# Optimization experiments

Hardware: AMD Instinct MI355X
Metric: run time of the kernel (lower is better)

The kernel has to match this reference:

```python
import jax, jax.numpy as jnp
import numpy as np

N = 100000
E = 1000000
P = 1000000
HID = 128
ROLE_VOCAB = 8
ROLE_DIM = 16
IDX_VOCAB = 1024
IDX_DIM = 8
FEAT = 14
IN_DIM = FEAT + IDX_DIM + ROLE_DIM  # 38


def setup_inputs() -> dict:
    key = jax.random.key(0)
    ks = jax.random.split(key, 20)
    s = 0.02
    return {
        "block_features": jax.random.normal(ks[0], (N, FEAT), jnp.float32),
        "role_ids": jax.random.randint(ks[1], (N,), 0, ROLE_VOCAB),
        "b2b_src": jax.random.randint(ks[2], (E,), 0, N),
        "b2b_dst": jax.random.randint(ks[3], (E,), 0, N),
        "b2b_w": jax.random.uniform(ks[4], (E,), jnp.float32),
        "p2b_block": jax.random.randint(ks[5], (P,), 0, N),
        "p2b_w": jax.random.uniform(ks[6], (P,), jnp.float32),
        "role_emb": jax.random.normal(ks[7], (ROLE_VOCAB, ROLE_DIM), jnp.float32),
        "idx_emb": jax.random.normal(ks[8], (IDX_VOCAB, IDX_DIM), jnp.float32),
        "W1": jax.random.normal(ks[9], (IN_DIM, HID), jnp.float32) * s,
        "b1": jnp.zeros((HID,), jnp.float32),
        "W2": jax.random.normal(ks[10], (HID, HID), jnp.float32) * s,
        "b2": jnp.zeros((HID,), jnp.float32),
        "M1": jax.random.normal(ks[11], (HID, HID), jnp.float32) * s,
        "mb1": jnp.zeros((HID,), jnp.float32),
        "M2": jax.random.normal(ks[12], (HID, HID), jnp.float32) * s,
        "mb2": jnp.zeros((HID,), jnp.float32),
        "ln_g": jnp.ones((HID,), jnp.float32),
        "ln_b": jnp.zeros((HID,), jnp.float32),
    }


def _layernorm(x, g, b, eps=1e-5):
    mu = jnp.mean(x, axis=-1, keepdims=True)
    var = jnp.mean(jnp.square(x - mu), axis=-1, keepdims=True)
    return (x - mu) * jax.lax.rsqrt(var + eps) * g + b


def reference(block_features, role_ids, b2b_src, b2b_dst, b2b_w, p2b_block, p2b_w,
              role_emb, idx_emb, W1, b1, W2, b2, M1, mb1, M2, mb2, ln_g, ln_b):
    n = block_features.shape[0]
    # embeddings + input MLP
    re = role_emb[role_ids]                                  # [N, 16]
    ie = idx_emb[jnp.arange(n) % IDX_VOCAB]                  # [N, 8]
    x = jnp.concatenate([block_features, re, ie], axis=-1)   # [N, 38]
    h = jax.nn.relu(x @ W1 + b1)
    emb = jax.nn.relu(h @ W2 + b2)                           # [N, HID]
    # b2b: symmetric weighted scatter-add of neighbor embeddings
    agg = jnp.zeros_like(emb)
    agg = agg.at[b2b_src].add(emb[b2b_dst] * b2b_w[:, None])
    agg = agg.at[b2b_dst].add(emb[b2b_src] * b2b_w[:, None])
    # p2b: agg[j] += emb[j] * w  ==  emb * (sum of pin weights per block)
    pw = jnp.zeros((n,), emb.dtype).at[p2b_block].add(p2b_w)
    agg = agg + emb * pw[:, None]
    # message MLP + residual + LayerNorm
    m = jax.nn.relu(agg @ M1 + mb1) @ M2 + mb2
    block_embeddings = _layernorm(emb + m, ln_g, ln_b)
    graph_embedding = jnp.mean(block_embeddings, axis=0)
    return block_embeddings, graph_embedding
```

## Files before the change

kernel.cpp:

```cpp
#include <hip/hip_runtime.h>

#define FEAT 14
#define ROLE_DIM 16
#define IDX_DIM 8
#define IN_DIM 38
#define HID 128
#define IDX_VOCAB 1024
#define BINN 128
#define NBINS_MAX 800
#define NSEG 1024
#define BINP_CAPT 8
#define BINP_SCAP 16
#define SORT_CAP 4096
#define SENT 0xFFFFFFFFu

typedef __attribute__((ext_vector_type(8))) short short8;
typedef __attribute__((ext_vector_type(4))) float f32x4;
typedef __attribute__((ext_vector_type(2))) float f32x2;

__device__ __forceinline__ ushort f2bf(float f) {
    uint u = __float_as_uint(f);
    return (ushort)((u + 0x7FFFu + ((u >> 16) & 1u)) >> 16);
}
__device__ __forceinline__ float bf2f(ushort h) {
    return __uint_as_float((uint)h << 16);
}
__device__ __forceinline__ uchar f2fp8(float f) {
    return (uchar)(__builtin_amdgcn_cvt_pk_fp8_f32(f, f, 0, false) & 0xff);
}

__global__ void k_prep(const float* __restrict__ W1, const float* __restrict__ W2,
                       const float* __restrict__ M1, const float* __restrict__ M2,
                       ushort* __restrict__ W1t, ushort* __restrict__ W2t,
                       ushort* __restrict__ M1t, ushort* __restrict__ M2t)
{
    int t = blockIdx.x * 256 + threadIdx.x;
    if (t < 8192) {
        int c = t >> 6, k = t & 63;
        W1t[t] = (k < IN_DIM) ? f2bf(W1[k * HID + c]) : (ushort)0;
    } else if (t < 24576) {
        int u = t - 8192; int c = u >> 7, k = u & 127;
        W2t[u] = f2bf(W2[k * HID + c]);
    } else if (t < 40960) {
        int u = t - 24576; int c = u >> 7, k = u & 127;
        M1t[u] = f2bf(M1[k * HID + c]);
    } else if (t < 57344) {
        int u = t - 40960; int c = u >> 7, k = u & 127;
        M2t[u] = f2bf(M2[k * HID + c]);
    }
}

#define LDSA 32768

__device__ __forceinline__ void embed_body(
    char* lds, int id,
    const float* __restrict__ feat, const int* __restrict__ role_ids,
    const float* __restrict__ role_emb, const float* __restrict__ idx_emb,
    const ushort* __restrict__ W1t, const float* __restrict__ b1,
    const ushort* __restrict__ W2t, const float* __restrict__ b2,
    ushort* __restrict__ embh, uchar* __restrict__ embf8, int N)
{
    const int tid = threadIdx.x;
    const int w = tid >> 6, l = tid & 63;
    const int li = l & 15, hi = l >> 4;
    const int base = id * 64;

    for (int c = 0; c < 4; ++c) {
        int idx = c * 256 + tid;
        int col = idx >> 3, ch = idx & 7;
        uint4 v = *(const uint4*)(W1t + col * 64 + ch * 8);
        *(uint4*)(lds + col * 256 + ((ch * 16) ^ ((col & 7) << 4))) = v;
    }
    {
        int row = tid >> 2, kq = (tid & 3) * 16;
        int gr = base + row; if (gr >= N) gr = N - 1;
        int rid = role_ids[gr];
        float xv[16];
        #pragma unroll
        for (int j = 0; j < 16; ++j) {
            int k = kq + j;
            float v = 0.0f;
            if (k < FEAT)                 v = feat[gr * FEAT + k];
            else if (k < FEAT + ROLE_DIM) v = role_emb[rid * ROLE_DIM + (k - FEAT)];
            else if (k < IN_DIM)          v = idx_emb[(gr & (IDX_VOCAB - 1)) * IDX_DIM + (k - FEAT - ROLE_DIM)];
            xv[j] = v;
        }
        uint p[8];
        #pragma unroll
        for (int j = 0; j < 8; ++j)
            p[j] = (uint)f2bf(xv[2 * j]) | ((uint)f2bf(xv[2 * j + 1]) << 16);
        char* db = lds + LDSA + row * 256;
        int sw = (row & 7) << 4;
        *(uint4*)(db + ((kq * 2) ^ sw))      = make_uint4(p[0], p[1], p[2], p[3]);
        *(uint4*)(db + ((kq * 2 + 16) ^ sw)) = make_uint4(p[4], p[5], p[6], p[7]);
    }
    __syncthreads();

    f32x4 C[8];
    #pragma unroll
    for (int ct = 0; ct < 8; ++ct) C[ct] = (f32x4){0.f, 0.f, 0.f, 0.f};
    {
        const int arow = w * 16 + li;
        const int asw = (arow & 7) << 4;
        #pragma unroll
        for (int ks = 0; ks < 2; ++ks) {
            short8 a = *(short8*)(lds + LDSA + arow * 256 + ((ks * 64 + hi * 16) ^ asw));
            #pragma unroll
            for (int ct = 0; ct < 8; ++ct) {
                int bcol = ct * 16 + li;
                short8 b = *(short8*)(lds + bcol * 256 + ((ks * 64 + hi * 16) ^ ((bcol & 7) << 4)));
                C[ct] = __builtin_amdgcn_mfma_f32_16x16x32_bf16(a, b, C[ct], 0, 0, 0);
            }
        }
    }
    __syncthreads();

    #pragma unroll
    for (int ct = 0; ct < 8; ++ct) {
        int col = ct * 16 + li;
        float bv = b1[col];
        #pragma unroll
        for (int r = 0; r < 4; ++r) {
            int hrow = w * 16 + hi * 4 + r;
            float h = fmaxf(C[ct][r] + bv, 0.0f);
            *(ushort*)(lds + LDSA + hrow * 256 + ((col * 2) ^ ((hrow & 7) << 4))) = f2bf(h);
        }
    }
    for (int c = 0; c < 8; ++c) {
        int idx = c * 256 + tid;
        int col = idx >> 4, ch = idx & 15;
        uint4 v = *(const uint4*)(W2t + col * 128 + ch * 8);
        *(uint4*)(lds + col * 256 + ((ch * 16) ^ ((col & 7) << 4))) = v;
    }
    __syncthreads();

    f32x4 C2[8];
    #pragma unroll
    for (int ct = 0; ct < 8; ++ct) C2[ct] = (f32x4){0.f, 0.f, 0.f, 0.f};
    {
        const int arow = w * 16 + li;
        const int asw = (arow & 7) << 4;
        #pragma unroll
        for (int ks = 0; ks < 4; ++ks) {
            short8 a = *(short8*)(lds + LDSA + arow * 256 + ((ks * 64 + hi * 16) ^ asw));
            #pragma unroll
            for (int ct = 0; ct < 8; ++ct) {
                int bcol = ct * 16 + li;
                short8 b = *(short8*)(lds + bcol * 256 + ((ks * 64 + hi * 16) ^ ((bcol & 7) << 4)));
                C2[ct] = __builtin_amdgcn_mfma_f32_16x16x32_bf16(a, b, C2[ct], 0, 0, 0);
            }
        }
    }

    #pragma unroll
    for (int ct = 0; ct < 8; ++ct) {
        int col = ct * 16 + li;
        float bv = b2[col];
        #pragma unroll
        for (int r = 0; r < 4; ++r) {
            int gr = base + w * 16 + hi * 4 + r;
            if (gr < N) {
                float o = fmaxf(C2[ct][r] + bv, 0.0f);
                embh[(size_t)gr * 128 + col] = f2bf(o);
                embf8[(size_t)gr * 128 + col] = f2fp8(o);
            }
        }
    }
}

__device__ __forceinline__ void binp_body(
    char* lds, int id,
    const int* __restrict__ src, const int* __restrict__ dst,
    const float* __restrict__ wgt, uint* __restrict__ staged,
    const int* __restrict__ pb, const float* __restrict__ pv,
    float* __restrict__ pw,
    int E, int P, int nbins, int chunkE, int chunkP)
{
    uint* buf   = (uint*)lds;
    int* curT   = (int*)(lds + 25600);
    const int tid = threadIdx.x;
    for (int i = tid; i < nbins; i += 256) curT[i] = 0;
    __syncthreads();

    const int lo = id * chunkE;
    const int hiE = (lo + chunkE) < E ? (lo + chunkE) : E;
    for (int i = lo + tid; i < hiE; i += 256) {
        int s = src[i], d = dst[i];
        uint q = (uint)(wgt[i] * 255.0f + 0.5f);
        int bs = s >> 7;
        uint es = ((uint)(s & 127) << 25) | ((uint)d << 8) | q;
        int ps = atomicAdd(&curT[bs], 1);
        if (ps < BINP_CAPT) buf[bs * BINP_CAPT + ps] = es;
        else if (ps < BINP_SCAP)
            staged[((size_t)bs * NSEG + id) * BINP_SCAP + ps] = es;
        int bd = d >> 7;
        uint ed = ((uint)(d & 127) << 25) | ((uint)s << 8) | q;
        int pd = atomicAdd(&curT[bd], 1);
        if (pd < BINP_CAPT) buf[bd * BINP_CAPT + pd] = ed;
        else if (pd < BINP_SCAP)
            staged[((size_t)bd * NSEG + id) * BINP_SCAP + pd] = ed;
    }
    __syncthreads();
    for (int b = tid; b < nbins; b += 256) {
        int tot = curT[b];
        int k = tot < BINP_CAPT ? tot : BINP_CAPT;
        uint* dp = staged + ((size_t)b * NSEG + id) * BINP_SCAP;
        for (int i = 0; i < k; ++i) dp[i] = buf[b * BINP_CAPT + i];
        if (tot < BINP_SCAP) dp[tot] = SENT;
    }

    int loP = id * chunkP;
    int hiP = loP + chunkP; if (hiP > P) hiP = P;
    for (int i = loP + tid; i < hiP; i += 256)
        atomicAdd(&pw[pb[i]], pv[i]);
}

__global__ __launch_bounds__(256) void k_embed_binp(
    const float* __restrict__ feat, const int* __restrict__ role_ids,
    const float* __restrict__ role_emb, const float* __restrict__ idx_emb,
    const ushort* __restrict__ W1t, const float* __restrict__ b1,
    const ushort* __restrict__ W2t, const float* __restrict__ b2,
    ushort* __restrict__ embh, uchar* __restrict__ embf8,
    const int* __restrict__ src, const int* __restrict__ dst,
    const float* __restrict__ wgt, uint* __restrict__ staged,
    const int* __restrict__ pb, const float* __restrict__ pv,
    float* __restrict__ pw,
    int N, int E, int P, int nbins, int chunkE, int chunkP)
{
    __shared__ char lds[49152];
    const int bid = blockIdx.x;
    int role, id;
    if (bid < 2 * NSEG) { role = bid & 1; id = bid >> 1; }
    else                { role = 0; id = NSEG + (bid - 2 * NSEG); }

    if (role == 0)
        embed_body(lds, id, feat, role_ids, role_emb, idx_emb,
                   W1t, b1, W2t, b2, embh, embf8, N);
    else
        binp_body(lds, id, src, dst, wgt, staged, pb, pv, pw,
                  E, P, nbins, chunkE, chunkP);
}

#define AREG 32768
#define WSUM 65536

__global__ __launch_bounds__(256) void k_agg_mlp(
    const uint* __restrict__ staged,
    const ushort* __restrict__ embh, const uchar* __restrict__ embf8,
    const float* __restrict__ pw,
    const ushort* __restrict__ M1t, const ushort* __restrict__ M2t,
    const float* __restrict__ mb1, const float* __restrict__ mb2,
    const float* __restrict__ ln_g, const float* __restrict__ ln_b,
    float* __restrict__ out, float* __restrict__ gsum, int N, int nbins)
{
    __shared__ char lds[67584];
    uint* sorted  = (uint*)lds;
    int*  hist    = (int*)(lds + 16384);
    int*  startL  = (int*)(lds + 16384 + 512);
    int*  curL    = (int*)(lds + 16384 + 1024);
    int*  sc      = (int*)(lds + 16384 + 1536);

    const int tid = threadIdx.x;
    const int b = blockIdx.x;
    const int baseNode = b << 7;
    const int w = tid >> 6, l = tid & 63;
    const int li = l & 15, hi = l >> 4;

    if (tid < BINN) hist[tid] = 0;
    __syncthreads();

    uint4 ent[4][4];
    int cSeg[4];
    #pragma unroll
    for (int ss = 0; ss < 4; ++ss) {
        int seg = ss * 256 + tid;
        const uint4* sp4 = (const uint4*)(staged + ((size_t)b * NSEG + seg) * BINP_SCAP);
        #pragma unroll
        for (int q = 0; q < 4; ++q) ent[ss][q] = sp4[q];
        int c = 16;
        #pragma unroll
        for (int q = 3; q >= 0; --q) {
            if (ent[ss][q].w == SENT) c = q * 4 + 3;
            if (ent[ss][q].z == SENT) c = q * 4 + 2;
            if (ent[ss][q].y == SENT) c = q * 4 + 1;
            if (ent[ss][q].x == SENT) c = q * 4 + 0;
        }
        cSeg[ss] = c;
    }
    #pragma unroll
    for (int ss = 0; ss < 4; ++ss) {
        int c = cSeg[ss];
        #pragma unroll
        for (int q = 0; q < 4; ++q) {
            uint e0 = ent[ss][q].x, e1 = ent[ss][q].y;
            uint e2 = ent[ss][q].z, e3 = ent[ss][q].w;
            if (q * 4 + 0 < c) atomicAdd(&hist[e0 >> 25], 1);
            if (q * 4 + 1 < c) atomicAdd(&hist[e1 >> 25], 1);
            if (q * 4 + 2 < c) atomicAdd(&hist[e2 >> 25], 1);
            if (q * 4 + 3 < c) atomicAdd(&hist[e3 >> 25], 1);
        }
    }
    __syncthreads();

    int v = (tid < BINN) ? hist[tid] : 0;
    if (tid < BINN) sc[tid] = v;
    __syncthreads();
    for (int off = 1; off < BINN; off <<= 1) {
        int u = (tid < BINN && tid >= off) ? sc[tid - off] : 0;
        __syncthreads();
        if (tid < BINN) sc[tid] += u;
        __syncthreads();
    }
    if (tid < BINN) {
        startL[tid] = sc[tid] - v;
        curL[tid]   = sc[tid] - v;
    }
    __syncthreads();

    #pragma unroll
    for (int ss = 0; ss < 4; ++ss) {
        int c = cSeg[ss];
        #pragma unroll
        for (int q = 0; q < 4; ++q) {
            uint ee[4] = {ent[ss][q].x, ent[ss][q].y, ent[ss][q].z, ent[ss][q].w};
            #pragma unroll
            for (int j = 0; j < 4; ++j) {
                if (q * 4 + j < c) {
                    uint e = ee[j];
                    int pos = atomicAdd(&curL[e >> 25], 1);
                    if (pos < SORT_CAP) sorted[pos] = e;
                }
            }
        }
    }
    __syncthreads();

    {
        const int g  = tid >> 3;
        const int cg = tid & 7;
        const int c0 = cg * 16;
        for (int h = 0; h < 4; ++h) {
            int nl = h * 32 + g;
            int node = baseNode + nl;
            uint p[8];
            if (node < N) {
                float acc[16];
                float pwn = pw[node];
                const uint4* r = (const uint4*)(embh + ((size_t)node << 7) + c0);
                uint4 u0 = r[0], u1 = r[1];
                uint uu[8] = {u0.x, u0.y, u0.z, u0.w, u1.x, u1.y, u1.z, u1.w};
                #pragma unroll
                for (int j = 0; j < 8; ++j) {
                    acc[2*j]   = __uint_as_float(uu[j] << 16) * pwn;
                    acc[2*j+1] = __uint_as_float(uu[j] & 0xffff0000u) * pwn;
                }
                const int st = startL[nl], deg = hist[nl];
                #pragma unroll 4
                for (int i = 0; i < deg; ++i) {
                    uint en = sorted[st + i];
                    int nb   = (int)((en >> 8) & 0x1FFFFu);
                    float wt = (float)(en & 255u) * (1.0f / 255.0f);
                    uint4 q = *(const uint4*)(embf8 + ((size_t)nb << 7) + c0);
                    uint qq[4] = {q.x, q.y, q.z, q.w};
                    #pragma unroll
                    for (int j = 0; j < 4; ++j) {
                        f32x2 lo = __builtin_amdgcn_cvt_pk_f32_fp8(qq[j], false);
                        f32x2 hi2 = __builtin_amdgcn_cvt_pk_f32_fp8(qq[j], true);
                        acc[4*j+0] = fmaf(lo.x,  wt, acc[4*j+0]);
                        acc[4*j+1] = fmaf(lo.y,  wt, acc[4*j+1]);
                        acc[4*j+2] = fmaf(hi2.x, wt, acc[4*j+2]);
                        acc[4*j+3] = fmaf(hi2.y, wt, acc[4*j+3]);
                    }
                }
                #pragma unroll
                for (int j = 0; j < 8; ++j)
                    p[j] = (uint)f2bf(acc[2*j]) | ((uint)f2bf(acc[2*j+1]) << 16);
            } else {
                #pragma unroll
                for (int j = 0; j < 8; ++j) p[j] = 0;
            }
            char* db = lds + AREG + nl * 256;
            int sw = (nl & 7) << 4;
            *(uint4*)(db + ((c0 * 2) ^ sw))      = make_uint4(p[0], p[1], p[2], p[3]);
            *(uint4*)(db + ((c0 * 2 + 16) ^ sw)) = make_uint4(p[4], p[5], p[6], p[7]);
        }
    }
    __syncthreads();

    for (int cc = 0; cc < 8; ++cc) {
        int idx = cc * 256 + tid;
        int col = idx >> 4, ch = idx & 15;
        uint4 vv = *(const uint4*)(M1t + col * 128 + ch * 8);
        *(uint4*)(lds + col * 256 + ((ch * 16) ^ ((col & 7) << 4))) = vv;
    }
    __syncthreads();

    #pragma unroll
    for (int h2 = 0; h2 < 2; ++h2) {
        f32x4 C1[8];
        #pragma unroll
        for (int ct = 0; ct < 8; ++ct) C1[ct] = (f32x4){0.f, 0.f, 0.f, 0.f};
        const int arow = h2 * 64 + w * 16 + li;
        const int asw = (arow & 7) << 4;
        #pragma unroll
        for (int ks = 0; ks < 4; ++ks) {
            short8 a = *(short8*)(lds + AREG + arow * 256 + ((ks * 64 + hi * 16) ^ asw));
            #pragma unroll
            for (int ct = 0; ct < 8; ++ct) {
                int bcol = ct * 16 + li;
                short8 bb = *(short8*)(lds + bcol * 256 + ((ks * 64 + hi * 16) ^ ((bcol & 7) << 4)));
                C1[ct] = __builtin_amdgcn_mfma_f32_16x16x32_bf16(a, bb, C1[ct], 0, 0, 0);
            }
        }
        #pragma unroll
        for (int ct = 0; ct < 8; ++ct) {
            int col = ct * 16 + li;
            float bv = mb1[col];
            #pragma unroll
            for (int r = 0; r < 4; ++r) {
                int hrow = h2 * 64 + w * 16 + hi * 4 + r;
                float h = fmaxf(C1[ct][r] + bv, 0.0f);
                *(ushort*)(lds + AREG + hrow * 256 + ((col * 2) ^ ((hrow & 7) << 4))) = f2bf(h);
            }
        }
    }
    __syncthreads();

    for (int cc = 0; cc < 8; ++cc) {
        int idx = cc * 256 + tid;
        int col = idx >> 4, ch = idx & 15;
        uint4 vv = *(const uint4*)(M2t + col * 128 + ch * 8);
        *(uint4*)(lds + col * 256 + ((ch * 16) ^ ((col & 7) << 4))) = vv;
    }
    __syncthreads();

    float cs[8];
    #pragma unroll
    for (int ct = 0; ct < 8; ++ct) cs[ct] = 0.0f;

    #pragma unroll
    for (int h2 = 0; h2 < 2; ++h2) {
        f32x4 C2[8];
        #pragma unroll
        for (int ct = 0; ct < 8; ++ct) C2[ct] = (f32x4){0.f, 0.f, 0.f, 0.f};
        const int arow = h2 * 64 + w * 16 + li;
        const int asw = (arow & 7) << 4;
        #pragma unroll
        for (int ks = 0; ks < 4; ++ks) {
            short8 a = *(short8*)(lds + AREG + arow * 256 + ((ks * 64 + hi * 16) ^ asw));
            #pragma unroll
            for (int ct = 0; ct < 8; ++ct) {
                int bcol = ct * 16 + li;
                short8 bb = *(short8*)(lds + bcol * 256 + ((ks * 64 + hi * 16) ^ ((bcol & 7) << 4)));
                C2[ct] = __builtin_amdgcn_mfma_f32_16x16x32_bf16(a, bb, C2[ct], 0, 0, 0);
            }
        }

        float y[8][4];
        #pragma unroll
        for (int ct = 0; ct < 8; ++ct) {
            int col = ct * 16 + li;
            float bv = mb2[col];
            #pragma unroll
            for (int r = 0; r < 4; ++r) {
                int gr = baseNode + h2 * 64 + w * 16 + hi * 4 + r;
                int grc = gr < N ? gr : N - 1;
                y[ct][r] = C2[ct][r] + bv + bf2f(embh[(size_t)grc * 128 + col]);
            }
        }
        float rs[4] = {0, 0, 0, 0}, rq[4] = {0, 0, 0, 0};
        #pragma unroll
        for (int ct = 0; ct < 8; ++ct)
            #pragma unroll
            for (int r = 0; r < 4; ++r) { rs[r] += y[ct][r]; rq[r] += y[ct][r] * y[ct][r]; }
        #pragma unroll
        for (int m = 1; m < 16; m <<= 1) {
            #pragma unroll
            for (int r = 0; r < 4; ++r) {
                rs[r] += __shfl_xor(rs[r], m);
                rq[r] += __shfl_xor(rq[r], m);
            }
        }
        float mu[4], rstd[4];
        #pragma unroll
        for (int r = 0; r < 4; ++r) {
            mu[r] = rs[r] * (1.0f / HID);
            float var = rq[r] * (1.0f / HID) - mu[r] * mu[r];
            rstd[r] = rsqrtf(var + 1e-5f);
        }
        #pragma unroll
        for (int ct = 0; ct < 8; ++ct) {
            int col = ct * 16 + li;
            float g = ln_g[col], bb2 = ln_b[col];
            #pragma unroll
            for (int r = 0; r < 4; ++r) {
                int gr = baseNode + h2 * 64 + w * 16 + hi * 4 + r;
                float o = (y[ct][r] - mu[r]) * rstd[r] * g + bb2;
                if (gr < N) {
                    out[(size_t)gr * 128 + col] = o;
                    cs[ct] += o;
                }
            }
        }
    }

    #pragma unroll
    for (int m = 16; m < 64; m <<= 1) {
        #pragma unroll
        for (int ct = 0; ct < 8; ++ct) cs[ct] += __shfl_xor(cs[ct], m);
    }
    float* wsum = (float*)(lds + WSUM);
    if (hi == 0) {
        #pragma unroll
        for (int ct = 0; ct < 8; ++ct) wsum[w * 128 + ct * 16 + li] = cs[ct];
    }
    __syncthreads();
    if (tid < 128) {
        float s = wsum[tid] + wsum[128 + tid] + wsum[256 + tid] + wsum[384 + tid];
        atomicAdd(&gsum[tid], s);
    }
}

__global__ void k_graph(const float* __restrict__ gsum, float* __restrict__ out,
                        int N)
{
    int j = threadIdx.x;
    out[(size_t)N * HID + j] = gsum[j] * (1.0f / (float)N);
}

extern "C" void kernel_launch(void* const* d_in, const int* in_sizes, int n_in,
                              void* d_out, int out_size, void* d_ws, size_t ws_size,
                              hipStream_t stream)
{
    const float* feat      = (const float*)d_in[0];
    const int*   role_ids  = (const int*)  d_in[1];
    const int*   b2b_src   = (const int*)  d_in[2];
    const int*   b2b_dst   = (const int*)  d_in[3];
    const float* b2b_w     = (const float*)d_in[4];
    const int*   p2b_block = (const int*)  d_in[5];
    const float* p2b_w     = (const float*)d_in[6];
    const float* role_emb  = (const float*)d_in[7];
    const float* idx_emb   = (const float*)d_in[8];
    const float* W1        = (const float*)d_in[9];
    const float* b1        = (const float*)d_in[10];
    const float* W2        = (const float*)d_in[11];
    const float* b2        = (const float*)d_in[12];
    const float* M1        = (const float*)d_in[13];
    const float* mb1       = (const float*)d_in[14];
    const float* M2        = (const float*)d_in[15];
    const float* mb2       = (const float*)d_in[16];
    const float* ln_g      = (const float*)d_in[17];
    const float* ln_b      = (const float*)d_in[18];

    const int N = in_sizes[1];
    const int E = in_sizes[2];
    const int P = in_sizes[5];

    float* out = (float*)d_out;

    const int nbins = (N + BINN - 1) >> 7;
    const int chunkE = (E + NSEG - 1) / NSEG;
    const int chunkP = (P + NSEG - 1) / NSEG;

    char* ws = (char*)d_ws;
    size_t embhBytes = (size_t)N * HID * sizeof(ushort);
    size_t embf8Bytes= (size_t)N * HID;
    size_t stagBytes = (size_t)nbins * NSEG * BINP_SCAP * sizeof(uint);
    size_t vecBytes  = (size_t)N * sizeof(float);

    ushort* embh    = (ushort*)ws;  ws += embhBytes;
    uchar*  embf8   = (uchar*)ws;   ws += embf8Bytes;
    uint*   staged  = (uint*)ws;    ws += stagBytes;
    float*  pw      = (float*)ws;   ws += vecBytes;
    float*  gsum    = (float*)ws;   ws += 512;
    ushort* W1t     = (ushort*)ws;  ws += 8192  * sizeof(ushort);
    ushort* W2t     = (ushort*)ws;  ws += 16384 * sizeof(ushort);
    ushort* M1t     = (ushort*)ws;  ws += 16384 * sizeof(ushort);
    ushort* M2t     = (ushort*)ws;  ws += 16384 * sizeof(ushort);

    hipMemsetAsync(pw, 0, vecBytes + 512, stream);

    const int nEmbed = (N + 63) / 64;

    k_prep<<<224, 256, 0, stream>>>(W1, W2, M1, M2, W1t, W2t, M1t, M2t);

    k_embed_binp<<<nEmbed + NSEG, 256, 0, stream>>>(
        feat, role_ids, role_emb, idx_emb, W1t, b1, W2t, b2, embh, embf8,
        b2b_src, b2b_dst, b2b_w, staged, p2b_block, p2b_w, pw,
        N, E, P, nbins, chunkE, chunkP);

    k_agg_mlp<<<nbins, 256, 0, stream>>>(
        staged, embh, embf8, pw, M1t, M2t, mb1, mb2, ln_g, ln_b,
        out, gsum, N, nbins);

    k_graph<<<1, HID, 0, stream>>>(gsum, out, N);
}
```

Before: 203.7 us.

## Shrink aggregation-MLP LDS footprint by staging weights in K-halves

The fused aggregation/MLP kernel no longer keeps a full 128x128 bf16 weight matrix in shared memory. It loads M1 and M2 in two 64-wide K halves into the region freed after sorting, moves the activation tile down, and reuses the auxiliary region for the final column sums. This cuts per-block LDS from about 66 KB to 50 KB so more blocks can be resident per CU, hiding the latency of the gather phase. In exchange, weights are reloaded once per 64-row half, and each K half adds two more block-wide barriers.

```diff
diff --git a/kernel.cpp b/kernel.cpp
--- a/kernel.cpp
+++ b/kernel.cpp
@@ -241,8 +241,8 @@
                   E, P, nbins, chunkE, chunkP);
 }
 
-#define AREG 32768
-#define WSUM 65536
+#define AOFF  18432
+#define AUXO  16384
 
 __global__ __launch_bounds__(256) void k_agg_mlp(
     const uint* __restrict__ staged,
@@ -253,12 +253,12 @@
     const float* __restrict__ ln_g, const float* __restrict__ ln_b,
     float* __restrict__ out, float* __restrict__ gsum, int N, int nbins)
 {
-    __shared__ char lds[67584];
+    __shared__ char lds[51200];
     uint* sorted  = (uint*)lds;
-    int*  hist    = (int*)(lds + 16384);
-    int*  startL  = (int*)(lds + 16384 + 512);
-    int*  curL    = (int*)(lds + 16384 + 1024);
-    int*  sc      = (int*)(lds + 16384 + 1536);
+    int*  hist    = (int*)(lds + AUXO);
+    int*  startL  = (int*)(lds + AUXO + 512);
+    int*  curL    = (int*)(lds + AUXO + 1024);
+    int*  sc      = (int*)(lds + AUXO + 1536);
 
     const int tid = threadIdx.x;
     const int b = blockIdx.x;
@@ -379,21 +379,12 @@
                 #pragma unroll
                 for (int j = 0; j < 8; ++j) p[j] = 0;
             }
-            char* db = lds + AREG + nl * 256;
+            char* db = lds + AOFF + nl * 256;
             int sw = (nl & 7) << 4;
             *(uint4*)(db + ((c0 * 2) ^ sw))      = make_uint4(p[0], p[1], p[2], p[3]);
             *(uint4*)(db + ((c0 * 2 + 16) ^ sw)) = make_uint4(p[4], p[5], p[6], p[7]);
         }
     }
-    __syncthreads();
-
-    for (int cc = 0; cc < 8; ++cc) {
-        int idx = cc * 256 + tid;
-        int col = idx >> 4, ch = idx & 15;
-        uint4 vv = *(const uint4*)(M1t + col * 128 + ch * 8);
-        *(uint4*)(lds + col * 256 + ((ch * 16) ^ ((col & 7) << 4))) = vv;
-    }
-    __syncthreads();
 
     #pragma unroll
     for (int h2 = 0; h2 < 2; ++h2) {
@@ -403,13 +394,25 @@
         const int arow = h2 * 64 + w * 16 + li;
         const int asw = (arow & 7) << 4;
         #pragma unroll
-        for (int ks = 0; ks < 4; ++ks) {
-            short8 a = *(short8*)(lds + AREG + arow * 256 + ((ks * 64 + hi * 16) ^ asw));
-            #pragma unroll
-            for (int ct = 0; ct < 8; ++ct) {
-                int bcol = ct * 16 + li;
-                short8 bb = *(short8*)(lds + bcol * 256 + ((ks * 64 + hi * 16) ^ ((bcol & 7) << 4)));
-                C1[ct] = __builtin_amdgcn_mfma_f32_16x16x32_bf16(a, bb, C1[ct], 0, 0, 0);
+        for (int kh = 0; kh < 2; ++kh) {
+            __syncthreads();
+            for (int cc = 0; cc < 4; ++cc) {
+                int idx = cc * 256 + tid;
+                int col = idx >> 3, ch = idx & 7;
+                uint4 vv = *(const uint4*)(M1t + col * 128 + kh * 64 + ch * 8);
+                *(uint4*)(lds + col * 128 + ((ch * 16) ^ ((col & 7) << 4))) = vv;
+            }
+            __syncthreads();
+            #pragma unroll
+            for (int ksh = 0; ksh < 2; ++ksh) {
+                int ks = kh * 2 + ksh;
+                short8 a = *(short8*)(lds + AOFF + arow * 256 + ((ks * 64 + hi * 16) ^ asw));
+                #pragma unroll
+                for (int ct = 0; ct < 8; ++ct) {
+                    int bcol = ct * 16 + li;
+                    short8 bb = *(short8*)(lds + bcol * 128 + ((ksh * 64 + hi * 16) ^ ((bcol & 7) << 4)));
+                    C1[ct] = __builtin_amdgcn_mfma_f32_16x16x32_bf16(a, bb, C1[ct], 0, 0, 0);
+                }
             }
         }
         #pragma unroll
@@ -420,19 +423,10 @@
             for (int r = 0; r < 4; ++r) {
                 int hrow = h2 * 64 + w * 16 + hi * 4 + r;
                 float h = fmaxf(C1[ct][r] + bv, 0.0f);
-                *(ushort*)(lds + AREG + hrow * 256 + ((col * 2) ^ ((hrow & 7) << 4))) = f2bf(h);
-            }
-        }
-    }
-    __syncthreads();
-
-    for (int cc = 0; cc < 8; ++cc) {
-        int idx = cc * 256 + tid;
-        int col = idx >> 4, ch = idx & 15;
-        uint4 vv = *(const uint4*)(M2t + col * 128 + ch * 8);
-        *(uint4*)(lds + col * 256 + ((ch * 16) ^ ((col & 7) << 4))) = vv;
-    }
-    __syncthreads();
+                *(ushort*)(lds + AOFF + hrow * 256 + ((col * 2) ^ ((hrow & 7) << 4))) = f2bf(h);
+            }
+        }
+    }
 
     float cs[8];
     #pragma unroll
@@ -446,13 +440,25 @@
         const int arow = h2 * 64 + w * 16 + li;
         const int asw = (arow & 7) << 4;
         #pragma unroll
-        for (int ks = 0; ks < 4; ++ks) {
-            short8 a = *(short8*)(lds + AREG + arow * 256 + ((ks * 64 + hi * 16) ^ asw));
-            #pragma unroll
-            for (int ct = 0; ct < 8; ++ct) {
-                int bcol = ct * 16 + li;
-                short8 bb = *(short8*)(lds + bcol * 256 + ((ks * 64 + hi * 16) ^ ((bcol & 7) << 4)));
-                C2[ct] = __builtin_amdgcn_mfma_f32_16x16x32_bf16(a, bb, C2[ct], 0, 0, 0);
+        for (int kh = 0; kh < 2; ++kh) {
+            __syncthreads();
+            for (int cc = 0; cc < 4; ++cc) {
+                int idx = cc * 256 + tid;
+                int col = idx >> 3, ch = idx & 7;
+                uint4 vv = *(const uint4*)(M2t + col * 128 + kh * 64 + ch * 8);
+                *(uint4*)(lds + col * 128 + ((ch * 16) ^ ((col & 7) << 4))) = vv;
+            }
+            __syncthreads();
+            #pragma unroll
+            for (int ksh = 0; ksh < 2; ++ksh) {
+                int ks = kh * 2 + ksh;
+                short8 a = *(short8*)(lds + AOFF + arow * 256 + ((ks * 64 + hi * 16) ^ asw));
+                #pragma unroll
+                for (int ct = 0; ct < 8; ++ct) {
+                    int bcol = ct * 16 + li;
+                    short8 bb = *(short8*)(lds + bcol * 128 + ((ksh * 64 + hi * 16) ^ ((bcol & 7) << 4)));
+                    C2[ct] = __builtin_amdgcn_mfma_f32_16x16x32_bf16(a, bb, C2[ct], 0, 0, 0);
+                }
             }
         }
 
@@ -509,7 +515,8 @@
         #pragma unroll
         for (int ct = 0; ct < 8; ++ct) cs[ct] += __shfl_xor(cs[ct], m);
     }
-    float* wsum = (float*)(lds + WSUM);
+    float* wsum = (float*)(lds + AUXO);
+    __syncthreads();
     if (hi == 0) {
         #pragma unroll
         for (int ct = 0; ct < 8; ++ct) wsum[w * 128 + ct * 16 + li] = cs[ct];
```

Result: faster. 193.6 us (median of 2 runs) (-4.9%).

## Halve node bins to 64 and stream MLP weights in K-chunks

Applied to the files above, without the earlier changes.

Node bins shrink from 128 to 64 nodes and the segment count from 1024 to 512. Edge entries now pack the local node index in the top 6 bits. The aggregation/MLP kernel handles 64 nodes per block and loads M1/M2 in 32-wide K slices instead of whole matrices, which cuts LDS per block from about 66KB to 25KB to allow higher occupancy. In exchange there are twice as many blocks, each reloading the weights, plus extra barriers per K slice.

```diff
diff --git a/kernel.cpp b/kernel.cpp
--- a/kernel.cpp
+++ b/kernel.cpp
@@ -6,12 +6,12 @@
 #define IN_DIM 38
 #define HID 128
 #define IDX_VOCAB 1024
-#define BINN 128
-#define NBINS_MAX 800
-#define NSEG 1024
-#define BINP_CAPT 8
+#define BINN 64
+#define NBINS_MAX 1600
+#define NSEG 512
+#define BINP_CAPT 6
 #define BINP_SCAP 16
-#define SORT_CAP 4096
+#define SORT_CAP 2048
 #define SENT 0xFFFFFFFFu
 
 typedef __attribute__((ext_vector_type(8))) short short8;
@@ -177,7 +177,7 @@
     int E, int P, int nbins, int chunkE, int chunkP)
 {
     uint* buf   = (uint*)lds;
-    int* curT   = (int*)(lds + 25600);
+    int* curT   = (int*)(lds + 38400);
     const int tid = threadIdx.x;
     for (int i = tid; i < nbins; i += 256) curT[i] = 0;
     __syncthreads();
@@ -187,14 +187,14 @@
     for (int i = lo + tid; i < hiE; i += 256) {
         int s = src[i], d = dst[i];
         uint q = (uint)(wgt[i] * 255.0f + 0.5f);
-        int bs = s >> 7;
-        uint es = ((uint)(s & 127) << 25) | ((uint)d << 8) | q;
+        int bs = s >> 6;
+        uint es = ((uint)(s & 63) << 26) | ((uint)d << 8) | q;
         int ps = atomicAdd(&curT[bs], 1);
         if (ps < BINP_CAPT) buf[bs * BINP_CAPT + ps] = es;
         else if (ps < BINP_SCAP)
             staged[((size_t)bs * NSEG + id) * BINP_SCAP + ps] = es;
-        int bd = d >> 7;
-        uint ed = ((uint)(d & 127) << 25) | ((uint)s << 8) | q;
+        int bd = d >> 6;
+        uint ed = ((uint)(d & 63) << 26) | ((uint)s << 8) | q;
         int pd = atomicAdd(&curT[bd], 1);
         if (pd < BINP_CAPT) buf[bd * BINP_CAPT + pd] = ed;
         else if (pd < BINP_SCAP)
@@ -241,8 +241,8 @@
                   E, P, nbins, chunkE, chunkP);
 }
 
-#define AREG 32768
-#define WSUM 65536
+#define AOFF  9216
+#define AUXO  8192
 
 __global__ __launch_bounds__(256) void k_agg_mlp(
     const uint* __restrict__ staged,
@@ -253,26 +253,26 @@
     const float* __restrict__ ln_g, const float* __restrict__ ln_b,
     float* __restrict__ out, float* __restrict__ gsum, int N, int nbins)
 {
-    __shared__ char lds[67584];
+    __shared__ char lds[25600];
     uint* sorted  = (uint*)lds;
-    int*  hist    = (int*)(lds + 16384);
-    int*  startL  = (int*)(lds + 16384 + 512);
-    int*  curL    = (int*)(lds + 16384 + 1024);
-    int*  sc      = (int*)(lds + 16384 + 1536);
+    int*  hist    = (int*)(lds + AUXO);
+    int*  startL  = (int*)(lds + AUXO + 256);
+    int*  curL    = (int*)(lds + AUXO + 512);
+    int*  sc      = (int*)(lds + AUXO + 768);
 
     const int tid = threadIdx.x;
     const int b = blockIdx.x;
-    const int baseNode = b << 7;
+    const int baseNode = b << 6;
     const int w = tid >> 6, l = tid & 63;
     const int li = l & 15, hi = l >> 4;
 
     if (tid < BINN) hist[tid] = 0;
     __syncthreads();
 
-    uint4 ent[4][4];
-    int cSeg[4];
-    #pragma unroll
-    for (int ss = 0; ss < 4; ++ss) {
+    uint4 ent[2][4];
+    int cSeg[2];
+    #pragma unroll
+    for (int ss = 0; ss < 2; ++ss) {
         int seg = ss * 256 + tid;
         const uint4* sp4 = (const uint4*)(staged + ((size_t)b * NSEG + seg) * BINP_SCAP);
         #pragma unroll
@@ -288,16 +288,16 @@
         cSeg[ss] = c;
     }
     #pragma unroll
-    for (int ss = 0; ss < 4; ++ss) {
+    for (int ss = 0; ss < 2; ++ss) {
         int c = cSeg[ss];
         #pragma unroll
         for (int q = 0; q < 4; ++q) {
             uint e0 = ent[ss][q].x, e1 = ent[ss][q].y;
             uint e2 = ent[ss][q].z, e3 = ent[ss][q].w;
-            if (q * 4 + 0 < c) atomicAdd(&hist[e0 >> 25], 1);
-            if (q * 4 + 1 < c) atomicAdd(&hist[e1 >> 25], 1);
-            if (q * 4 + 2 < c) atomicAdd(&hist[e2 >> 25], 1);
-            if (q * 4 + 3 < c) atomicAdd(&hist[e3 >> 25], 1);
+            if (q * 4 + 0 < c) atomicAdd(&hist[e0 >> 26], 1);
+            if (q * 4 + 1 < c) atomicAdd(&hist[e1 >> 26], 1);
+            if (q * 4 + 2 < c) atomicAdd(&hist[e2 >> 26], 1);
+            if (q * 4 + 3 < c) atomicAdd(&hist[e3 >> 26], 1);
         }
     }
     __syncthreads();
@@ -318,7 +318,7 @@
     __syncthreads();
 
     #pragma unroll
-    for (int ss = 0; ss < 4; ++ss) {
+    for (int ss = 0; ss < 2; ++ss) {
         int c = cSeg[ss];
         #pragma unroll
         for (int q = 0; q < 4; ++q) {
@@ -327,7 +327,7 @@
             for (int j = 0; j < 4; ++j) {
                 if (q * 4 + j < c) {
                     uint e = ee[j];
-                    int pos = atomicAdd(&curL[e >> 25], 1);
+                    int pos = atomicAdd(&curL[e >> 26], 1);
                     if (pos < SORT_CAP) sorted[pos] = e;
                 }
             }
@@ -339,7 +339,7 @@
         const int g  = tid >> 3;
         const int cg = tid & 7;
         const int c0 = cg * 16;
-        for (int h = 0; h < 4; ++h) {
+        for (int h = 0; h < 2; ++h) {
             int nl = h * 32 + g;
             int node = baseNode + nl;
             uint p[8];
@@ -379,129 +379,119 @@
                 #pragma unroll
                 for (int j = 0; j < 8; ++j) p[j] = 0;
             }
-            char* db = lds + AREG + nl * 256;
+            char* db = lds + AOFF + nl * 256;
             int sw = (nl & 7) << 4;
             *(uint4*)(db + ((c0 * 2) ^ sw))      = make_uint4(p[0], p[1], p[2], p[3]);
             *(uint4*)(db + ((c0 * 2 + 16) ^ sw)) = make_uint4(p[4], p[5], p[6], p[7]);
         }
     }
-    __syncthreads();
-
-    for (int cc = 0; cc < 8; ++cc) {
-        int idx = cc * 256 + tid;
-        int col = idx >> 4, ch = idx & 15;
-        uint4 vv = *(const uint4*)(M1t + col * 128 + ch * 8);
-        *(uint4*)(lds + col * 256 + ((ch * 16) ^ ((col & 7) << 4))) = vv;
-    }
-    __syncthreads();
-
-    #pragma unroll
-    for (int h2 = 0; h2 < 2; ++h2) {
-        f32x4 C1[8];
-        #pragma unroll
-        for (int ct = 0; ct < 8; ++ct) C1[ct] = (f32x4){0.f, 0.f, 0.f, 0.f};
-        const int arow = h2 * 64 + w * 16 + li;
-        const int asw = (arow & 7) << 4;
-        #pragma unroll
-        for (int ks = 0; ks < 4; ++ks) {
-            short8 a = *(short8*)(lds + AREG + arow * 256 + ((ks * 64 + hi * 16) ^ asw));
-            #pragma unroll
-            for (int ct = 0; ct < 8; ++ct) {
-                int bcol = ct * 16 + li;
-                short8 bb = *(short8*)(lds + bcol * 256 + ((ks * 64 + hi * 16) ^ ((bcol & 7) << 4)));
-                C1[ct] = __builtin_amdgcn_mfma_f32_16x16x32_bf16(a, bb, C1[ct], 0, 0, 0);
+
+    const int arow = w * 16 + li;
+    const int asw  = (arow & 7) << 4;
+
+    f32x4 C1[8];
+    #pragma unroll
+    for (int ct = 0; ct < 8; ++ct) C1[ct] = (f32x4){0.f, 0.f, 0.f, 0.f};
+    #pragma unroll
+    for (int kq = 0; kq < 4; ++kq) {
+        __syncthreads();
+        for (int cc = 0; cc < 2; ++cc) {
+            int idx = cc * 256 + tid;
+            int col = idx >> 2, ch = idx & 3;
+            uint4 vv = *(const uint4*)(M1t + col * 128 + kq * 32 + ch * 8);
+            *(uint4*)(lds + col * 64 + ch * 16) = vv;
+        }
+        __syncthreads();
+        short8 a = *(short8*)(lds + AOFF + arow * 256 + ((kq * 64 + hi * 16) ^ asw));
+        #pragma unroll
+        for (int ct = 0; ct < 8; ++ct) {
+            int bcol = ct * 16 + li;
+            short8 bb = *(short8*)(lds + bcol * 64 + hi * 16);
+            C1[ct] = __builtin_amdgcn_mfma_f32_16x16x32_bf16(a, bb, C1[ct], 0, 0, 0);
+        }
+    }
+    __syncthreads();
+    #pragma unroll
+    for (int ct = 0; ct < 8; ++ct) {
+        int col = ct * 16 + li;
+        float bv = mb1[col];
+        #pragma unroll
+        for (int r = 0; r < 4; ++r) {
+            int hrow = w * 16 + hi * 4 + r;
+            float h = fmaxf(C1[ct][r] + bv, 0.0f);
+            *(ushort*)(lds + AOFF + hrow * 256 + ((col * 2) ^ ((hrow & 7) << 4))) = f2bf(h);
+        }
+    }
+
+    f32x4 C2[8];
+    #pragma unroll
+    for (int ct = 0; ct < 8; ++ct) C2[ct] = (f32x4){0.f, 0.f, 0.f, 0.f};
+    #pragma unroll
+    for (int kq = 0; kq < 4; ++kq) {
+        __syncthreads();
+        for (int cc = 0; cc < 2; ++cc) {
+            int idx = cc * 256 + tid;
+            int col = idx >> 2, ch = idx & 3;
+            uint4 vv = *(const uint4*)(M2t + col * 128 + kq * 32 + ch * 8);
+            *(uint4*)(lds + col * 64 + ch * 16) = vv;
+        }
+        __syncthreads();
+        short8 a = *(short8*)(lds + AOFF + arow * 256 + ((kq * 64 + hi * 16) ^ asw));
+        #pragma unroll
+        for (int ct = 0; ct < 8; ++ct) {
+            int bcol = ct * 16 + li;
+            short8 bb = *(short8*)(lds + bcol * 64 + hi * 16);
+            C2[ct] = __builtin_amdgcn_mfma_f32_16x16x32_bf16(a, bb, C2[ct], 0, 0, 0);
+        }
+    }
+
+    float y[8][4];
+    #pragma unroll
+    for (int ct = 0; ct < 8; ++ct) {
+        int col = ct * 16 + li;
+        float bv = mb2[col];
+        #pragma unroll
+        for (int r = 0; r < 4; ++r) {
+            int gr = baseNode + w * 16 + hi * 4 + r;
+            int grc = gr < N ? gr : N - 1;
+            y[ct][r] = C2[ct][r] + bv + bf2f(embh[(size_t)grc * 128 + col]);
+        }
+    }
+    float rs[4] = {0, 0, 0, 0}, rq[4] = {0, 0, 0, 0};
+    #pragma unroll
+    for (int ct = 0; ct < 8; ++ct)
+        #pragma unroll
+        for (int r = 0; r < 4; ++r) { rs[r] += y[ct][r]; rq[r] += y[ct][r] * y[ct][r]; }
+    #pragma unroll
+    for (int m = 1; m < 16; m <<= 1) {
+        #pragma unroll
+        for (int r = 0; r < 4; ++r) {
+            rs[r] += __shfl_xor(rs[r], m);
+            rq[r] += __shfl_xor(rq[r], m);
+        }
+    }
+    float mu[4], rstd[4];
+    #pragma unroll
+    for (int r = 0; r < 4; ++r) {
+        mu[r] = rs[r] * (1.0f / HID);
+        float var = rq[r] * (1.0f / HID) - mu[r] * mu[r];
+        rstd[r] = rsqrtf(var + 1e-5f);
+    }
+    float cs[8];
+    #pragma unroll
+    for (int ct = 0; ct < 8; ++ct) {
+        cs[ct] = 0.0f;
+        int col = ct * 16 + li;
+        float g = ln_g[col], bb2 = ln_b[col];
+        #pragma unroll
+        for (int r = 0; r < 4; ++r) {
+            int gr = baseNode + w * 16 + hi * 4 + r;
+            float o = (y[ct][r] - mu[r]) * rstd[r] * g + bb2;
+            if (gr < N) {
+                out[(size_t)gr * 128 + col] = o;
+                cs[ct] += o;
             }
         }
-        #pragma unroll
-        for (int ct = 0; ct < 8; ++ct) {
-            int col = ct * 16 + li;
-            float bv = mb1[col];
-            #pragma unroll
-            for (int r = 0; r < 4; ++r) {
-                int hrow = h2 * 64 + w * 16 + hi * 4 + r;
-                float h = fmaxf(C1[ct][r] + bv, 0.0f);
-                *(ushort*)(lds + AREG + hrow * 256 + ((col * 2) ^ ((hrow & 7) << 4))) = f2bf(h);
-            }
-        }
-    }
-    __syncthreads();
-
-    for (int cc = 0; cc < 8; ++cc) {
-        int idx = cc * 256 + tid;
-        int col = idx >> 4, ch = idx & 15;
-        uint4 vv = *(const uint4*)(M2t + col * 128 + ch * 8);
-        *(uint4*)(lds + col * 256 + ((ch * 16) ^ ((col & 7) << 4))) = vv;
-    }
-    __syncthreads();
-
-    float cs[8];
-    #pragma unroll
-    for (int ct = 0; ct < 8; ++ct) cs[ct] = 0.0f;
-
-    #pragma unroll
-    for (int h2 = 0; h2 < 2; ++h2) {
-        f32x4 C2[8];
-        #pragma unroll
-        for (int ct = 0; ct < 8; ++ct) C2[ct] = (f32x4){0.f, 0.f, 0.f, 0.f};
-        const int arow = h2 * 64 + w * 16 + li;
-        const int asw = (arow & 7) << 4;
-        #pragma unroll
-        for (int ks = 0; ks < 4; ++ks) {
-            short8 a = *(short8*)(lds + AREG + arow * 256 + ((ks * 64 + hi * 16) ^ asw));
-            #pragma unroll
-            for (int ct = 0; ct < 8; ++ct) {
-                int bcol = ct * 16 + li;
-                short8 bb = *(short8*)(lds + bcol * 256 + ((ks * 64 + hi * 16) ^ ((bcol & 7) << 4)));
-                C2[ct] = __builtin_amdgcn_mfma_f32_16x16x32_bf16(a, bb, C2[ct], 0, 0, 0);
-            }
-        }
-
-        float y[8][4];
-        #pragma unroll
-        for (int ct = 0; ct < 8; ++ct) {
-            int col = ct * 16 + li;
-            float bv = mb2[col];
-            #pragma unroll
-            for (int r = 0; r < 4; ++r) {
-                int gr = baseNode + h2 * 64 + w * 16 + hi * 4 + r;
-                int grc = gr < N ? gr : N - 1;
-                y[ct][r] = C2[ct][r] + bv + bf2f(embh[(size_t)grc * 128 + col]);
-            }
-        }
-        float rs[4] = {0, 0, 0, 0}, rq[4] = {0, 0, 0, 0};
-        #pragma unroll
-        for (int ct = 0; ct < 8; ++ct)
-            #pragma unroll
-            for (int r = 0; r < 4; ++r) { rs[r] += y[ct][r]; rq[r] += y[ct][r] * y[ct][r]; }
-        #pragma unroll
-        for (int m = 1; m < 16; m <<= 1) {
-            #pragma unroll
-            for (int r = 0; r < 4; ++r) {
-                rs[r] += __shfl_xor(rs[r], m);
-                rq[r] += __shfl_xor(rq[r], m);
-            }
-        }
-        float mu[4], rstd[4];
-        #pragma unroll
-        for (int r = 0; r < 4; ++r) {
-            mu[r] = rs[r] * (1.0f / HID);
-            float var = rq[r] * (1.0f / HID) - mu[r] * mu[r];
-            rstd[r] = rsqrtf(var + 1e-5f);
-        }
-        #pragma unroll
-        for (int ct = 0; ct < 8; ++ct) {
-            int col = ct * 16 + li;
-            float g = ln_g[col], bb2 = ln_b[col];
-            #pragma unroll
-            for (int r = 0; r < 4; ++r) {
-                int gr = baseNode + h2 * 64 + w * 16 + hi * 4 + r;
-                float o = (y[ct][r] - mu[r]) * rstd[r] * g + bb2;
-                if (gr < N) {
-                    out[(size_t)gr * 128 + col] = o;
-                    cs[ct] += o;
-                }
-            }
-        }
     }
 
     #pragma unroll
@@ -509,7 +499,8 @@
         #pragma unroll
         for (int ct = 0; ct < 8; ++ct) cs[ct] += __shfl_xor(cs[ct], m);
     }
-    float* wsum = (float*)(lds + WSUM);
+    float* wsum = (float*)lds;
+    __syncthreads();
     if (hi == 0) {
         #pragma unroll
         for (int ct = 0; ct < 8; ++ct) wsum[w * 128 + ct * 16 + li] = cs[ct];
@@ -558,7 +549,7 @@
 
     float* out = (float*)d_out;
 
-    const int nbins = (N + BINN - 1) >> 7;
+    const int nbins = (N + BINN - 1) >> 6;
     const int chunkE = (E + NSEG - 1) / NSEG;
     const int chunkP = (P + NSEG - 1) / NSEG;
 
```

Result: faster. 199.5 us (-2.1%).
